# Optimization experiments

Hardware: AMD Instinct MI355X
Metric: run time of the kernel (lower is better)

The kernel has to match this reference:

```python
import jax, jax.numpy as jnp
import numpy as np
from jax import lax

B, N0, N1 = 4, 256, 256
NVOX = N0 * N1
NSUB, NLOR, RAYLEN, NTOF = 8, 32768, 256, 1
NBLK, CH = 4, 16
SUBSETS = np.linspace(0, NSUB, NBLK, endpoint=False).astype(int)  # [0,2,4,6]


def setup_inputs() -> dict:
    key = jax.random.key(0)
    ks = jax.random.split(key, 12)
    osem = jax.random.uniform(ks[0], (B, 1, N0, N1, 1), jnp.float32) + 0.1
    data = jax.random.uniform(ks[1], (B, NSUB, NLOR, NTOF), jnp.float32)
    mult = jax.random.uniform(ks[2], (B, NSUB, NLOR, 1), jnp.float32) + 0.5
    contam = jax.random.uniform(ks[3], (B, NSUB, NLOR, NTOF), jnp.float32) + 0.1
    adjoint_ones = jax.random.uniform(ks[4], (B, NSUB, N0, N1, 1), jnp.float32) + 0.5
    norm = jax.random.uniform(ks[5], (B,), jnp.float32) + 0.5
    ray_idx = jax.random.randint(ks[6], (NSUB, NLOR, RAYLEN), 0, NVOX, dtype=jnp.int32)
    proj_weights = jax.random.uniform(ks[7], (NSUB, NLOR, RAYLEN), jnp.float32) / RAYLEN
    w1 = jax.random.normal(ks[8], (CH, 1, 3, 3), jnp.float32) * 0.05
    b1 = jnp.zeros((CH,), jnp.float32)
    w2 = jax.random.normal(ks[9], (1, CH, 3, 3), jnp.float32) * 0.05
    b2 = jnp.zeros((1,), jnp.float32)
    net_weight = jnp.asarray(1.0, jnp.float32)
    return dict(osem=osem, data=data, multiplicative_corrections=mult,
                contamination=contam, adjoint_ones=adjoint_ones, norm=norm,
                ray_idx=ray_idx, proj_weights=proj_weights,
                w1=w1, b1=b1, w2=w2, b2=b2, net_weight=net_weight)


def _conv(x, w):
    return lax.conv_general_dilated(x, w, (1, 1), 'SAME',
                                    dimension_numbers=('NCHW', 'OIHW', 'NCHW'))


def _net(x, w1, b1, w2, b2):
    # x: (B,1,N0,N1,1) -> treat as NCHW 2D image with 1 channel
    img = x[:, :, :, :, 0]
    h = jax.nn.relu(_conv(img, w1) + b1[None, :, None, None])
    o = _conv(h, w2) + b2[None, :, None, None]
    return o[..., None]


def _fidelity(x, data, mult, contam, adj_ones, norm, ray_idx, pw, subset):
    # unscaled image, flattened: (B, NVOX)
    img_flat = norm[:, None] * x[:, 0, :, :, 0].reshape(B, NVOX)
    ii = ray_idx[subset]          # (NLOR, RAYLEN) voxel indices per ray
    ww = pw[subset]               # (NLOR, RAYLEN) Joseph weights
    # forward projection: gather + weighted sum along each ray
    fwd = jnp.einsum('bls,ls->bl', img_flat[:, ii], ww)[..., None]  # (B,NLOR,1)
    expected = mult[:, subset] * fwd + contam[:, subset]            # (B,NLOR,NTOF)
    ratio = (mult[:, subset] * (1.0 - data[:, subset] / expected)).sum(-1)  # (B,NLOR)
    # adjoint projection: scatter-add along each ray
    back = jnp.zeros((B, NVOX), x.dtype).at[:, ii].add(ww * ratio[:, :, None])
    upd = back * (img_flat / adj_ones[:, subset].reshape(B, NVOX))
    return (upd / norm[:, None]).reshape(B, 1, N0, N1, 1)


def reference(osem, data, multiplicative_corrections, contamination,
              adjoint_ones, norm, ray_idx, proj_weights,
              w1, b1, w2, b2, net_weight):
    x = osem
    for subset in SUBSETS:
        x_data = _fidelity(x, data, multiplicative_corrections, contamination,
                           adjoint_ones, norm, ray_idx, proj_weights, int(subset))
        x_net = _net(x, w1, b1, w2, b2)
        x = jax.nn.relu(osem - x_data + net_weight * x_net)
    return x
```

## Files before the change

kernel.cpp:

```cpp
#include <hip/hip_runtime.h>
#include <hip/hip_fp16.h>

#define BB 4
#define N0 256
#define N1 256
#define NVOX 65536
#define NSUB 8
#define NLOR 32768
#define RAYLEN 256
#define CH 16
#define NPTS (NLOR * RAYLEN)
#define VOXQ 16384
#define VOXT 32768
#define CCH 32

__global__ __launch_bounds__(256) void k_transpose(const float* __restrict__ osem,
                                                   float* __restrict__ xt) {
    int v = blockIdx.x * blockDim.x + threadIdx.x;
    if (v >= NVOX) return;
    float4 o;
    o.x = osem[0 * NVOX + v];
    o.y = osem[1 * NVOX + v];
    o.z = osem[2 * NVOX + v];
    o.w = osem[3 * NVOX + v];
    ((float4*)xt)[v] = o;
}

__device__ __forceinline__ float upk_w(unsigned p) {
    return __half2float(__ushort_as_half((unsigned short)(p >> 16)));
}

__device__ __forceinline__ unsigned pk2(float a, float b) {
    __half2 h = __floats2half2_rn(a, b);
    return *reinterpret_cast<unsigned*>(&h);
}

__global__ __launch_bounds__(256) void k_fwdpack(
    const int* __restrict__ ridx,
    const float* __restrict__ pw,
    const float* __restrict__ xt,
    const float* __restrict__ data,
    const float* __restrict__ mult,
    const float* __restrict__ contam,
    const float* __restrict__ norm,
    float* __restrict__ ratio,
    unsigned* __restrict__ packed)
{
    const int wave = threadIdx.x >> 6;
    const int lane = threadIdx.x & 63;
    const int half = lane >> 5;
    const int sub  = lane & 31;
    const int l = blockIdx.x * 8 + wave * 2 + half;
    const long e0 = (long)l * 64;

    const long ea = e0 + sub;
    const long eb = e0 + sub + 32;

    int4   ida = ((const int4*)ridx)[ea];
    float4 wa  = ((const float4*)pw)[ea];
    int4   idb = ((const int4*)ridx)[eb];
    float4 wb  = ((const float4*)pw)[eb];

    uint4 pka, pkb;
    pka.x = (unsigned)ida.x | ((unsigned)__half_as_ushort(__float2half_rn(wa.x)) << 16);
    pka.y = (unsigned)ida.y | ((unsigned)__half_as_ushort(__float2half_rn(wa.y)) << 16);
    pka.z = (unsigned)ida.z | ((unsigned)__half_as_ushort(__float2half_rn(wa.z)) << 16);
    pka.w = (unsigned)ida.w | ((unsigned)__half_as_ushort(__float2half_rn(wa.w)) << 16);
    pkb.x = (unsigned)idb.x | ((unsigned)__half_as_ushort(__float2half_rn(wb.x)) << 16);
    pkb.y = (unsigned)idb.y | ((unsigned)__half_as_ushort(__float2half_rn(wb.y)) << 16);
    pkb.z = (unsigned)idb.z | ((unsigned)__half_as_ushort(__float2half_rn(wb.z)) << 16);
    pkb.w = (unsigned)idb.w | ((unsigned)__half_as_ushort(__float2half_rn(wb.w)) << 16);
    ((uint4*)packed)[ea] = pka;
    ((uint4*)packed)[eb] = pkb;

    float ax = 0.f, ay = 0.f, az = 0.f, aw = 0.f;
    {
        float4 xv;
        xv = ((const float4*)xt)[ida.x];
        ax += xv.x * wa.x; ay += xv.y * wa.x; az += xv.z * wa.x; aw += xv.w * wa.x;
        xv = ((const float4*)xt)[ida.y];
        ax += xv.x * wa.y; ay += xv.y * wa.y; az += xv.z * wa.y; aw += xv.w * wa.y;
        xv = ((const float4*)xt)[ida.z];
        ax += xv.x * wa.z; ay += xv.y * wa.z; az += xv.z * wa.z; aw += xv.w * wa.z;
        xv = ((const float4*)xt)[ida.w];
        ax += xv.x * wa.w; ay += xv.y * wa.w; az += xv.z * wa.w; aw += xv.w * wa.w;
        xv = ((const float4*)xt)[idb.x];
        ax += xv.x * wb.x; ay += xv.y * wb.x; az += xv.z * wb.x; aw += xv.w * wb.x;
        xv = ((const float4*)xt)[idb.y];
        ax += xv.x * wb.y; ay += xv.y * wb.y; az += xv.z * wb.y; aw += xv.w * wb.y;
        xv = ((const float4*)xt)[idb.z];
        ax += xv.x * wb.z; ay += xv.y * wb.z; az += xv.z * wb.z; aw += xv.w * wb.z;
        xv = ((const float4*)xt)[idb.w];
        ax += xv.x * wb.w; ay += xv.y * wb.w; az += xv.z * wb.w; aw += xv.w * wb.w;
    }
#pragma unroll
    for (int off = 16; off >= 1; off >>= 1) {
        ax += __shfl_xor(ax, off);
        ay += __shfl_xor(ay, off);
        az += __shfl_xor(az, off);
        aw += __shfl_xor(aw, off);
    }
    if (sub == 0) {
        float fwd[4] = {ax, ay, az, aw};
        float rr[4];
#pragma unroll
        for (int b = 0; b < 4; ++b) {
            long o = (long)b * (NSUB * NLOR) + l;
            float m = mult[o];
            float ee = m * (norm[b] * fwd[b]) + contam[o];
            rr[b] = m * (1.0f - data[o] / ee);
        }
        ((float4*)ratio)[l] = make_float4(rr[0], rr[1], rr[2], rr[3]);
    }
}

__global__ __launch_bounds__(1024) void k_back_pk(
    const unsigned* __restrict__ packed,
    const float* __restrict__ ratio,
    unsigned* __restrict__ part,
    int PC)
{
    __shared__ unsigned acc[VOXQ];
    const int c = blockIdx.x;
    const int g = blockIdx.y;
    const int p = g & 1;
    const unsigned lo = (unsigned)(g >> 1) * VOXQ;

    for (int q = threadIdx.x; q < VOXQ; q += 1024) acc[q] = 0u;
    __syncthreads();

    const unsigned abase = (unsigned)(uintptr_t)(&acc[0]);

    const int n4 = PC >> 2;
    const uint4* src = (const uint4*)packed + (size_t)c * n4;
    const float2* rat2 = (const float2*)ratio;
    const int e0 = c * n4;

#define PKADD(u, R)                                                              \
    {                                                                            \
        unsigned q_ = ((u) & 0xffffu) - lo;                                      \
        if (q_ < VOXQ) {                                                         \
            float w_ = upk_w(u);                                                 \
            unsigned d_ = pk2(w_ * (R).x, w_ * (R).y);                           \
            unsigned a_ = abase + (q_ << 2);                                     \
            asm volatile("ds_pk_add_f16 %0, %1" :: "v"(a_), "v"(d_) : "memory"); \
        }                                                                        \
    }
#define PROC(P, R) PKADD(P.x, R) PKADD(P.y, R) PKADD(P.z, R) PKADD(P.w, R)

    for (int base4 = 0; base4 < n4; base4 += 4096) {
        const int ea = base4 + (int)threadIdx.x;
        uint4 A = src[ea];
        uint4 B = src[ea + 1024];
        uint4 C2 = src[ea + 2048];
        uint4 D = src[ea + 3072];
        float2 ra = rat2[(((e0 + ea) >> 6) << 1) + p];
        float2 rb = rat2[(((e0 + ea + 1024) >> 6) << 1) + p];
        float2 rc = rat2[(((e0 + ea + 2048) >> 6) << 1) + p];
        float2 rd = rat2[(((e0 + ea + 3072) >> 6) << 1) + p];
        PROC(A, ra) PROC(B, rb) PROC(C2, rc) PROC(D, rd)
    }
#undef PROC
#undef PKADD

    asm volatile("s_waitcnt lgkmcnt(0)" ::: "memory");
    __syncthreads();

    unsigned* dst = part + ((size_t)c * 2 + p) * NVOX + lo;
    for (int q = threadIdx.x; q < VOXQ; q += 1024) dst[q] = acc[q];
}

__global__ __launch_bounds__(256) void k_reduce(
    const unsigned* __restrict__ part,
    float* __restrict__ back)
{
    const int t = blockIdx.x * 256 + threadIdx.x;
    const int v0 = t * 2;
    const int pr = blockIdx.y;
    float s0 = 0.f, s1 = 0.f, s2 = 0.f, s3 = 0.f;
#pragma unroll
    for (int cc = 0; cc < CCH; ++cc) {
        uint2 u = *(const uint2*)&part[((size_t)cc * 2 + pr) * NVOX + v0];
        s0 += __half2float(__ushort_as_half((unsigned short)(u.x & 0xffffu)));
        s1 += __half2float(__ushort_as_half((unsigned short)(u.x >> 16)));
        s2 += __half2float(__ushort_as_half((unsigned short)(u.y & 0xffffu)));
        s3 += __half2float(__ushort_as_half((unsigned short)(u.y >> 16)));
    }
    ((float2*)back)[(size_t)v0 * 2 + pr] = make_float2(s0, s1);
    ((float2*)back)[(size_t)(v0 + 1) * 2 + pr] = make_float2(s2, s3);
}

#define TI 8
#define TJ 32
__global__ __launch_bounds__(256) void k_net_combine(
    const float* __restrict__ xt_in,
    const float* __restrict__ w1,
    const float* __restrict__ b1,
    const float* __restrict__ w2,
    const float* __restrict__ b2,
    const float* __restrict__ back,
    const float* __restrict__ osem,
    const float* __restrict__ adj,
    const float* __restrict__ nwp,
    float* __restrict__ xt_out,
    float* __restrict__ out_planar)
{
    __shared__ float img[(TI + 4) * (TJ + 4)];
    __shared__ float hsm[8 * (TI + 2) * (TJ + 2)];
    __shared__ float ws1[144], ws2[144], bs1[16];

    const int i0 = blockIdx.x * TI;
    const int j0 = blockIdx.y * TJ;
    const int b  = blockIdx.z;
    const int tid = threadIdx.x;

    if (tid < 144) { ws1[tid] = w1[tid]; ws2[tid] = w2[tid]; }
    if (tid < 16) bs1[tid] = b1[tid];

    for (int q = tid; q < (TI + 4) * (TJ + 4); q += 256) {
        int ii = q / (TJ + 4), jj = q % (TJ + 4);
        int gi = i0 - 2 + ii, gj = j0 - 2 + jj;
        float v = 0.f;
        if (gi >= 0 && gi < N0 && gj >= 0 && gj < N1)
            v = xt_in[(size_t)(gi * N1 + gj) * 4 + b];
        img[q] = v;
    }
    __syncthreads();

    const int li = tid >> 5, lj = tid & 31;
    const int HA = (TI + 2) * (TJ + 2);
    float o = b2[0];

#pragma unroll
    for (int pass = 0; pass < 2; ++pass) {
        for (int q = tid; q < 8 * HA; q += 256) {
            int c8 = q / HA, r = q % HA;
            int c = pass * 8 + c8;
            int ii = r / (TJ + 2), jj = r % (TJ + 2);
            int gi = i0 - 1 + ii, gj = j0 - 1 + jj;
            float hv = 0.f;
            if (gi >= 0 && gi < N0 && gj >= 0 && gj < N1) {
                float a = bs1[c];
#pragma unroll
                for (int di = 0; di < 3; ++di)
#pragma unroll
                    for (int dj = 0; dj < 3; ++dj)
                        a += img[(ii + di) * (TJ + 4) + (jj + dj)] *
                             ws1[c * 9 + di * 3 + dj];
                hv = fmaxf(a, 0.f);
            }
            hsm[q] = hv;
        }
        __syncthreads();
#pragma unroll
        for (int c8 = 0; c8 < 8; ++c8)
#pragma unroll
            for (int di = 0; di < 3; ++di)
#pragma unroll
                for (int dj = 0; dj < 3; ++dj)
                    o += hsm[c8 * HA + (li + di) * (TJ + 2) + (lj + dj)] *
                         ws2[(pass * 8 + c8) * 9 + di * 3 + dj];
        if (pass == 0) __syncthreads();
    }

    const float nw = nwp[0];
    const int pr = b >> 1, hi = b & 1;
    const int v = (i0 + li) * N1 + (j0 + lj);
    float2 bp = ((const float2*)back)[(size_t)v * 2 + pr];
    float bk = hi ? bp.y : bp.x;
    float xv = img[(li + 2) * (TJ + 4) + (lj + 2)];
    float x_data = bk * xv / adj[(size_t)b * NSUB * NVOX + v];
    float xnew = fmaxf(osem[(size_t)b * NVOX + v] - x_data + nw * o, 0.f);
    xt_out[(size_t)v * 4 + b] = xnew;
    if (out_planar) out_planar[(size_t)b * NVOX + v] = xnew;
}

__global__ __launch_bounds__(256) void k_fwd(
    const int* __restrict__ ridx, const float* __restrict__ pw,
    const float* __restrict__ xt, const float* __restrict__ data,
    const float* __restrict__ mult, const float* __restrict__ contam,
    const float* __restrict__ norm, float* __restrict__ ratio)
{
    const int wave = threadIdx.x >> 6;
    const int lane = threadIdx.x & 63;
    const int l = blockIdx.x * 4 + wave;
    const long base = (long)l * RAYLEN;
    float ax = 0.f, ay = 0.f, az = 0.f, aw = 0.f;
#pragma unroll
    for (int k = 0; k < 4; ++k) {
        int r = lane + (k << 6);
        float wt = pw[base + r];
        float4 xv = ((const float4*)xt)[ridx[base + r]];
        ax += xv.x * wt; ay += xv.y * wt; az += xv.z * wt; aw += xv.w * wt;
    }
#pragma unroll
    for (int off = 32; off >= 1; off >>= 1) {
        ax += __shfl_xor(ax, off); ay += __shfl_xor(ay, off);
        az += __shfl_xor(az, off); aw += __shfl_xor(aw, off);
    }
    if (lane == 0) {
        float fwd[4] = {ax, ay, az, aw};
        float rr[4];
#pragma unroll
        for (int b = 0; b < 4; ++b) {
            long o = (long)b * (NSUB * NLOR) + l;
            float m = mult[o];
            float e = m * (norm[b] * fwd[b]) + contam[o];
            rr[b] = m * (1.0f - data[o] / e);
        }
        ((float4*)ratio)[l] = make_float4(rr[0], rr[1], rr[2], rr[3]);
    }
}

__global__ __launch_bounds__(1024) void k_back(
    const int* __restrict__ ridx, const float* __restrict__ pw,
    const float* __restrict__ ratio, float* __restrict__ part, int PC)
{
    __shared__ float acc[VOXT];
    const int c = blockIdx.x;
    const int g = blockIdx.y;
    const int b = g & 3;
    const int lo = (g >> 2) * VOXT;
    for (int q = threadIdx.x; q < VOXT; q += 1024) acc[q] = 0.0f;
    __syncthreads();
    const int pbeg = c * PC;
    const int pend = min(pbeg + PC, NPTS);
#pragma unroll 2
    for (int pt = pbeg + (int)threadIdx.x * 4; pt < pend; pt += 1024 * 4) {
        int4   id = *(const int4*)(ridx + pt);
        float4 w  = *(const float4*)(pw + pt);
        float  r  = ratio[(pt >> 8) * 4 + b];
        unsigned r0 = (unsigned)(id.x - lo), r1 = (unsigned)(id.y - lo);
        unsigned r2 = (unsigned)(id.z - lo), r3 = (unsigned)(id.w - lo);
        if (r0 < VOXT) atomicAdd(&acc[r0], w.x * r);
        if (r1 < VOXT) atomicAdd(&acc[r1], w.y * r);
        if (r2 < VOXT) atomicAdd(&acc[r2], w.z * r);
        if (r3 < VOXT) atomicAdd(&acc[r3], w.w * r);
    }
    __syncthreads();
    float4* dst = (float4*)(part + ((size_t)c * 4 + b) * NVOX + lo);
    const float4* srcl = (const float4*)acc;
    for (int q = threadIdx.x; q < VOXT / 4; q += 1024) dst[q] = srcl[q];
}

__global__ __launch_bounds__(256) void k_conv1(
    const float* __restrict__ xt, const float* __restrict__ w1,
    const float* __restrict__ b1, float* __restrict__ h)
{
    int t = blockIdx.x * blockDim.x + threadIdx.x;
    int b = t >> 16;
    int v = t & 65535;
    int i = v >> 8, j = v & 255;
    float in[3][3];
#pragma unroll
    for (int di = 0; di < 3; ++di)
#pragma unroll
        for (int dj = 0; dj < 3; ++dj) {
            int ii = i + di - 1, jj = j + dj - 1;
            in[di][dj] = (ii >= 0 && ii < N0 && jj >= 0 && jj < N1)
                             ? xt[(size_t)((ii << 8) | jj) * 4 + b]
                             : 0.0f;
        }
    float* hp = h + (size_t)t * CH;
#pragma unroll
    for (int c = 0; c < CH; ++c) {
        float acc = b1[c];
#pragma unroll
        for (int di = 0; di < 3; ++di)
#pragma unroll
            for (int dj = 0; dj < 3; ++dj)
                acc += in[di][dj] * w1[c * 9 + di * 3 + dj];
        hp[c] = fmaxf(acc, 0.0f);
    }
}

__global__ __launch_bounds__(256) void k_combine(
    const float* __restrict__ h, const float* __restrict__ w2,
    const float* __restrict__ b2, const float* __restrict__ part,
    const float* __restrict__ xt_in, const float* __restrict__ osem,
    const float* __restrict__ adj, const float* __restrict__ nwp, int C,
    float* __restrict__ xt_out, float* __restrict__ out_planar)
{
    int t = blockIdx.x * blockDim.x + threadIdx.x;
    int b = t >> 16;
    int v = t & 65535;
    int i = v >> 8, j = v & 255;
    float o = b2[0];
#pragma unroll
    for (int di = 0; di < 3; ++di) {
        int ii = i + di - 1;
        if (ii < 0 || ii >= N0) continue;
#pragma unroll
        for (int dj = 0; dj < 3; ++dj) {
            int jj = j + dj - 1;
            if (jj < 0 || jj >= N1) continue;
            const float* hp = h + ((size_t)b * NVOX + ((ii << 8) | jj)) * CH;
#pragma unroll
            for (int c = 0; c < CH; ++c)
                o += hp[c] * w2[c * 9 + di * 3 + dj];
        }
    }
    float bk = 0.0f;
    for (int c = 0; c < C; ++c)
        bk += part[((size_t)c * 4 + b) * NVOX + v];
    float xv = xt_in[(size_t)v * 4 + b];
    float x_data = bk * xv / adj[(size_t)b * NSUB * NVOX + v];
    float xnew = osem[t] - x_data + nwp[0] * o;
    xnew = fmaxf(xnew, 0.0f);
    xt_out[(size_t)v * 4 + b] = xnew;
    if (out_planar) out_planar[t] = xnew;
}

extern "C" void kernel_launch(void* const* d_in, const int* in_sizes, int n_in,
                              void* d_out, int out_size, void* d_ws, size_t ws_size,
                              hipStream_t stream) {
    const float* osem   = (const float*)d_in[0];
    const float* data   = (const float*)d_in[1];
    const float* mult   = (const float*)d_in[2];
    const float* contam = (const float*)d_in[3];
    const float* adj    = (const float*)d_in[4];
    const float* norm   = (const float*)d_in[5];
    const int*   ray_idx = (const int*)d_in[6];
    const float* pw     = (const float*)d_in[7];
    const float* w1     = (const float*)d_in[8];
    const float* b1     = (const float*)d_in[9];
    const float* w2     = (const float*)d_in[10];
    const float* b2     = (const float*)d_in[11];
    const float* nw     = (const float*)d_in[12];
    float* out = (float*)d_out;

    const size_t MB = 1024 * 1024;
    float* ws  = (float*)d_ws;
    float* xtA = ws;
    float* xtB = ws + (size_t)NVOX * 4;
    const int subsets[4] = {0, 2, 4, 6};

    bool use_pk = (ws_size >= 90 * MB);

    k_transpose<<<NVOX / 256, 256, 0, stream>>>(osem, xtA);

    if (use_pk) {
        const int PC = NPTS / CCH;
        unsigned* part   = (unsigned*)(ws + (size_t)NVOX * 8);
        unsigned* packed = part + (size_t)CCH * 2 * NVOX;
        float*    backv  = (float*)(packed + (size_t)NPTS);
        float*    ratio  = backv + (size_t)NVOX * 4;

        float* xin = xtA;
        float* xout = xtB;
        for (int it = 0; it < 4; ++it) {
            int s = subsets[it];
            k_fwdpack<<<NLOR / 8, 256, 0, stream>>>(
                ray_idx + (size_t)s * NPTS, pw + (size_t)s * NPTS, xin,
                data + (size_t)s * NLOR, mult + (size_t)s * NLOR,
                contam + (size_t)s * NLOR, norm, ratio, packed);
            k_back_pk<<<dim3(CCH, 8), 1024, 0, stream>>>(packed, ratio, part, PC);
            k_reduce<<<dim3(NVOX / 512, 2), 256, 0, stream>>>(part, backv);
            k_net_combine<<<dim3(N0 / TI, N1 / TJ, BB), 256, 0, stream>>>(
                xin, w1, b1, w2, b2, backv, osem,
                adj + (size_t)s * NVOX, nw,
                xout, (it == 3) ? out : nullptr);
            float* tmp = xin; xin = xout; xout = tmp;
        }
    } else {
        int C = (ws_size >= (18 + 32) * MB + NVOX) ? 32
              : (ws_size >= (18 + 16) * MB + NVOX) ? 16 : 8;
        const int PC = NPTS / C;
        float* part = ws + (size_t)NVOX * 8;
        float* h    = part + (size_t)C * NVOX * 4;
        float* ratio = h;

        float* xin = xtA;
        float* xout = xtB;
        for (int it = 0; it < 4; ++it) {
            int s = subsets[it];
            const int*   rs = ray_idx + (size_t)s * NPTS;
            const float* ps = pw + (size_t)s * NPTS;
            k_fwd<<<NLOR / 4, 256, 0, stream>>>(
                rs, ps, xin,
                data + (size_t)s * NLOR, mult + (size_t)s * NLOR,
                contam + (size_t)s * NLOR, norm, ratio);
            k_back<<<dim3(C, 8), 1024, 0, stream>>>(rs, ps, ratio, part, PC);
            k_conv1<<<(BB * NVOX) / 256, 256, 0, stream>>>(xin, w1, b1, h);
            k_combine<<<(BB * NVOX) / 256, 256, 0, stream>>>(
                h, w2, b2, part, xin, osem,
                adj + (size_t)s * NVOX, nw, C,
                xout, (it == 3) ? out : nullptr);
            float* tmp = xin; xin = xout; xout = tmp;
        }
    }
}
```

Measured before the change: 663.0 us.

## Fuse all iteration stages into one persistent kernel with grid-wide barriers

Replaces the per-iteration chain of forward-pack, LDS back-projection, reduce and net-combine kernels with a single persistent kernel of 256×1024-thread blocks. Stages are separated by a hand-rolled atomic grid barrier, and the initial transpose is folded in as well. The aim is to remove the launch gaps and kernel tail effects across the 17 launches. In exchange, the forward gather runs at a fixed occupancy of one 1024-thread block per CU with a loop of 4 rays per wave. The code also assumes every block is co-resident, and the barrier will deadlock if they are not.

```diff
diff --git a/kernel.cpp b/kernel.cpp
--- a/kernel.cpp
+++ b/kernel.cpp
@@ -13,6 +13,291 @@
 #define VOXQ 16384
 #define VOXT 32768
 #define CCH 32
+#define NBLK 256
+#define NTHR 1024
+
+__device__ __forceinline__ float upk_w(unsigned p) {
+    return __half2float(__ushort_as_half((unsigned short)(p >> 16)));
+}
+__device__ __forceinline__ unsigned pk2(float a, float b) {
+    __half2 h = __floats2half2_rn(a, b);
+    return *reinterpret_cast<unsigned*>(&h);
+}
+
+__global__ __launch_bounds__(1024, 4) void k_mega(
+    const float* __restrict__ osem,
+    const float* __restrict__ data,
+    const float* __restrict__ mult,
+    const float* __restrict__ contam,
+    const float* __restrict__ adj,
+    const float* __restrict__ norm,
+    const int*   __restrict__ ray_idx,
+    const float* __restrict__ pw,
+    const float* __restrict__ w1, const float* __restrict__ b1,
+    const float* __restrict__ w2, const float* __restrict__ b2,
+    const float* __restrict__ nwp,
+    float* __restrict__ xtA, float* __restrict__ xtB,
+    unsigned* __restrict__ part,
+    unsigned* __restrict__ packed,
+    float* __restrict__ backv,
+    float* __restrict__ ratio,
+    int* __restrict__ bar,
+    float* __restrict__ out)
+{
+    __shared__ unsigned lds[16384];
+    const int bid = blockIdx.x;
+    const int tid = threadIdx.x;
+    int barph = 0;
+
+    auto gbar = [&]() {
+        __syncthreads();
+        if (tid == 0) {
+            ++barph;
+            __hip_atomic_fetch_add(&bar[0], 1, __ATOMIC_RELEASE,
+                                   __HIP_MEMORY_SCOPE_AGENT);
+            const int target = NBLK * barph;
+            while (__hip_atomic_load(&bar[0], __ATOMIC_RELAXED,
+                                     __HIP_MEMORY_SCOPE_AGENT) < target)
+                __builtin_amdgcn_s_sleep(8);
+            (void)__hip_atomic_load(&bar[0], __ATOMIC_ACQUIRE,
+                                    __HIP_MEMORY_SCOPE_AGENT);
+        }
+        __syncthreads();
+    };
+
+    {
+        int t = bid * NTHR + tid;
+        if (t < NVOX) {
+            float4 o;
+            o.x = osem[t];
+            o.y = osem[NVOX + t];
+            o.z = osem[2 * NVOX + t];
+            o.w = osem[3 * NVOX + t];
+            ((float4*)xtA)[t] = o;
+        }
+    }
+    gbar();
+
+    float* xin = xtA;
+    float* xout = xtB;
+    for (int it = 0; it < 4; ++it) {
+        const int s = it * 2;
+        const int*   rs = ray_idx + (size_t)s * NPTS;
+        const float* ps = pw + (size_t)s * NPTS;
+
+        {
+            const int wv = bid * 16 + (tid >> 6);
+            const int lane = tid & 63;
+            const int half = lane >> 5;
+            const int sub = lane & 31;
+            for (int k = 0; k < 4; ++k) {
+                const int l = wv * 8 + k * 2 + half;
+                const long e0 = (long)l * 64;
+                const long ea = e0 + sub, eb = e0 + sub + 32;
+
+                int4   ida = ((const int4*)rs)[ea];
+                float4 wa  = ((const float4*)ps)[ea];
+                int4   idb = ((const int4*)rs)[eb];
+                float4 wb  = ((const float4*)ps)[eb];
+
+                uint4 pka, pkb;
+                pka.x = (unsigned)ida.x | ((unsigned)__half_as_ushort(__float2half_rn(wa.x)) << 16);
+                pka.y = (unsigned)ida.y | ((unsigned)__half_as_ushort(__float2half_rn(wa.y)) << 16);
+                pka.z = (unsigned)ida.z | ((unsigned)__half_as_ushort(__float2half_rn(wa.z)) << 16);
+                pka.w = (unsigned)ida.w | ((unsigned)__half_as_ushort(__float2half_rn(wa.w)) << 16);
+                pkb.x = (unsigned)idb.x | ((unsigned)__half_as_ushort(__float2half_rn(wb.x)) << 16);
+                pkb.y = (unsigned)idb.y | ((unsigned)__half_as_ushort(__float2half_rn(wb.y)) << 16);
+                pkb.z = (unsigned)idb.z | ((unsigned)__half_as_ushort(__float2half_rn(wb.z)) << 16);
+                pkb.w = (unsigned)idb.w | ((unsigned)__half_as_ushort(__float2half_rn(wb.w)) << 16);
+                ((uint4*)packed)[ea] = pka;
+                ((uint4*)packed)[eb] = pkb;
+
+                float ax = 0.f, ay = 0.f, az = 0.f, aw = 0.f;
+                float4 xv;
+                xv = ((const float4*)xin)[ida.x];
+                ax += xv.x * wa.x; ay += xv.y * wa.x; az += xv.z * wa.x; aw += xv.w * wa.x;
+                xv = ((const float4*)xin)[ida.y];
+                ax += xv.x * wa.y; ay += xv.y * wa.y; az += xv.z * wa.y; aw += xv.w * wa.y;
+                xv = ((const float4*)xin)[ida.z];
+                ax += xv.x * wa.z; ay += xv.y * wa.z; az += xv.z * wa.z; aw += xv.w * wa.z;
+                xv = ((const float4*)xin)[ida.w];
+                ax += xv.x * wa.w; ay += xv.y * wa.w; az += xv.z * wa.w; aw += xv.w * wa.w;
+                xv = ((const float4*)xin)[idb.x];
+                ax += xv.x * wb.x; ay += xv.y * wb.x; az += xv.z * wb.x; aw += xv.w * wb.x;
+                xv = ((const float4*)xin)[idb.y];
+                ax += xv.x * wb.y; ay += xv.y * wb.y; az += xv.z * wb.y; aw += xv.w * wb.y;
+                xv = ((const float4*)xin)[idb.z];
+                ax += xv.x * wb.z; ay += xv.y * wb.z; az += xv.z * wb.z; aw += xv.w * wb.z;
+                xv = ((const float4*)xin)[idb.w];
+                ax += xv.x * wb.w; ay += xv.y * wb.w; az += xv.z * wb.w; aw += xv.w * wb.w;
+
+#pragma unroll
+                for (int off = 16; off >= 1; off >>= 1) {
+                    ax += __shfl_xor(ax, off);
+                    ay += __shfl_xor(ay, off);
+                    az += __shfl_xor(az, off);
+                    aw += __shfl_xor(aw, off);
+                }
+                if (sub == 0) {
+                    float fwd[4] = {ax, ay, az, aw};
+                    float rr[4];
+#pragma unroll
+                    for (int b = 0; b < 4; ++b) {
+                        long o = (long)b * (NSUB * NLOR) + (long)s * NLOR + l;
+                        float m = mult[o];
+                        float ee = m * (norm[b] * fwd[b]) + contam[o];
+                        rr[b] = m * (1.0f - data[o] / ee);
+                    }
+                    ((float4*)ratio)[l] = make_float4(rr[0], rr[1], rr[2], rr[3]);
+                }
+            }
+        }
+        gbar();
+
+        {
+            const int c = bid >> 3;
+            const int g = bid & 7;
+            const int p = g & 1;
+            const unsigned lo = (unsigned)(g >> 1) * VOXQ;
+
+            for (int q = tid; q < VOXQ; q += NTHR) lds[q] = 0u;
+            __syncthreads();
+
+            const unsigned abase = (unsigned)(uintptr_t)(&lds[0]);
+            const int n4 = (NPTS / CCH) >> 2;
+            const uint4* src = (const uint4*)packed + (size_t)c * n4;
+            const float2* rat2 = (const float2*)ratio;
+            const int e0 = c * n4;
+
+#define PKADD(u, R)                                                              \
+    {                                                                            \
+        unsigned q_ = ((u) & 0xffffu) - lo;                                      \
+        if (q_ < VOXQ) {                                                         \
+            float w_ = upk_w(u);                                                 \
+            unsigned d_ = pk2(w_ * (R).x, w_ * (R).y);                           \
+            unsigned a_ = abase + (q_ << 2);                                     \
+            asm volatile("ds_pk_add_f16 %0, %1" :: "v"(a_), "v"(d_) : "memory"); \
+        }                                                                        \
+    }
+#define PROC(P, R) PKADD(P.x, R) PKADD(P.y, R) PKADD(P.z, R) PKADD(P.w, R)
+
+            for (int base4 = 0; base4 < n4; base4 += 4096) {
+                const int ea = base4 + tid;
+                uint4 A = src[ea];
+                uint4 B = src[ea + 1024];
+                uint4 C2 = src[ea + 2048];
+                uint4 D = src[ea + 3072];
+                float2 ra = rat2[(((e0 + ea) >> 6) << 1) + p];
+                float2 rb = rat2[(((e0 + ea + 1024) >> 6) << 1) + p];
+                float2 rc = rat2[(((e0 + ea + 2048) >> 6) << 1) + p];
+                float2 rd = rat2[(((e0 + ea + 3072) >> 6) << 1) + p];
+                PROC(A, ra) PROC(B, rb) PROC(C2, rc) PROC(D, rd)
+            }
+#undef PROC
+#undef PKADD
+            asm volatile("s_waitcnt lgkmcnt(0)" ::: "memory");
+            __syncthreads();
+
+            unsigned* dst = part + ((size_t)c * 2 + p) * NVOX + lo;
+            for (int q = tid; q < VOXQ; q += NTHR) dst[q] = lds[q];
+        }
+        gbar();
+
+        {
+            int t = bid * NTHR + tid;
+            if (t < 2 * NVOX) {
+                int pr = t >> 16;
+                int v = t & 65535;
+                float s0 = 0.f, s1 = 0.f;
+#pragma unroll
+                for (int cc = 0; cc < CCH; ++cc) {
+                    unsigned u = part[((size_t)cc * 2 + pr) * NVOX + v];
+                    s0 += __half2float(__ushort_as_half((unsigned short)(u & 0xffffu)));
+                    s1 += __half2float(__ushort_as_half((unsigned short)(u >> 16)));
+                }
+                ((float2*)backv)[(size_t)v * 2 + pr] = make_float2(s0, s1);
+            }
+        }
+        gbar();
+
+        {
+            const int sb = tid >> 8, stid = tid & 255;
+            const int T = bid * 4 + sb;
+            const int b = T >> 8;
+            const int rem = T & 255;
+            const int i0 = (rem >> 3) * 8;
+            const int j0 = (rem & 7) * 32;
+
+            float* img = (float*)lds + sb * 432;
+            float* hsm = (float*)lds + 1728 + sb * 2720;
+            float* wsh = (float*)lds + 1728 + 4 * 2720;
+            float* ws1 = wsh;
+            float* ws2 = wsh + 144;
+            float* bs1 = wsh + 288;
+            if (tid < 144) { ws1[tid] = w1[tid]; ws2[tid] = w2[tid]; }
+            if (tid < 16) bs1[tid] = b1[tid];
+
+            for (int q = stid; q < 432; q += 256) {
+                int ii = q / 36, jj = q % 36;
+                int gi = i0 - 2 + ii, gj = j0 - 2 + jj;
+                float v = 0.f;
+                if (gi >= 0 && gi < N0 && gj >= 0 && gj < N1)
+                    v = xin[(size_t)(gi * N1 + gj) * 4 + b];
+                img[q] = v;
+            }
+            __syncthreads();
+
+            const int HA = 10 * 34;
+            const int li = stid >> 5, lj = stid & 31;
+            float o = b2[0];
+#pragma unroll
+            for (int pass = 0; pass < 2; ++pass) {
+                for (int q = stid; q < 8 * HA; q += 256) {
+                    int c8 = q / HA, r = q % HA;
+                    int c = pass * 8 + c8;
+                    int ii = r / 34, jj = r % 34;
+                    int gi = i0 - 1 + ii, gj = j0 - 1 + jj;
+                    float hv = 0.f;
+                    if (gi >= 0 && gi < N0 && gj >= 0 && gj < N1) {
+                        float a = bs1[c];
+#pragma unroll
+                        for (int di = 0; di < 3; ++di)
+#pragma unroll
+                            for (int dj = 0; dj < 3; ++dj)
+                                a += img[(ii + di) * 36 + (jj + dj)] *
+                                     ws1[c * 9 + di * 3 + dj];
+                        hv = fmaxf(a, 0.f);
+                    }
+                    hsm[q] = hv;
+                }
+                __syncthreads();
+#pragma unroll
+                for (int c8 = 0; c8 < 8; ++c8)
+#pragma unroll
+                    for (int di = 0; di < 3; ++di)
+#pragma unroll
+                        for (int dj = 0; dj < 3; ++dj)
+                            o += hsm[c8 * HA + (li + di) * 34 + (lj + dj)] *
+                                 ws2[(pass * 8 + c8) * 9 + di * 3 + dj];
+                if (pass == 0) __syncthreads();
+            }
+
+            const float nw = nwp[0];
+            const int pr = b >> 1, hi = b & 1;
+            const int v = (i0 + li) * N1 + (j0 + lj);
+            float2 bp = ((const float2*)backv)[(size_t)v * 2 + pr];
+            float bk = hi ? bp.y : bp.x;
+            float xv = img[(li + 2) * 36 + (lj + 2)];
+            float x_data = bk * xv / adj[(size_t)b * NSUB * NVOX + (size_t)s * NVOX + v];
+            float xnew = fmaxf(osem[(size_t)b * NVOX + v] - x_data + nw * o, 0.f);
+            xout[(size_t)v * 4 + b] = xnew;
+            if (it == 3) out[(size_t)b * NVOX + v] = xnew;
+        }
+        gbar();
+
+        float* tmp = xin; xin = xout; xout = tmp;
+    }
+}
 
 __global__ __launch_bounds__(256) void k_transpose(const float* __restrict__ osem,
                                                    float* __restrict__ xt) {
@@ -24,255 +309,6 @@
     o.z = osem[2 * NVOX + v];
     o.w = osem[3 * NVOX + v];
     ((float4*)xt)[v] = o;
-}
-
-__device__ __forceinline__ float upk_w(unsigned p) {
-    return __half2float(__ushort_as_half((unsigned short)(p >> 16)));
-}
-
-__device__ __forceinline__ unsigned pk2(float a, float b) {
-    __half2 h = __floats2half2_rn(a, b);
-    return *reinterpret_cast<unsigned*>(&h);
-}
-
-__global__ __launch_bounds__(256) void k_fwdpack(
-    const int* __restrict__ ridx,
-    const float* __restrict__ pw,
-    const float* __restrict__ xt,
-    const float* __restrict__ data,
-    const float* __restrict__ mult,
-    const float* __restrict__ contam,
-    const float* __restrict__ norm,
-    float* __restrict__ ratio,
-    unsigned* __restrict__ packed)
-{
-    const int wave = threadIdx.x >> 6;
-    const int lane = threadIdx.x & 63;
-    const int half = lane >> 5;
-    const int sub  = lane & 31;
-    const int l = blockIdx.x * 8 + wave * 2 + half;
-    const long e0 = (long)l * 64;
-
-    const long ea = e0 + sub;
-    const long eb = e0 + sub + 32;
-
-    int4   ida = ((const int4*)ridx)[ea];
-    float4 wa  = ((const float4*)pw)[ea];
-    int4   idb = ((const int4*)ridx)[eb];
-    float4 wb  = ((const float4*)pw)[eb];
-
-    uint4 pka, pkb;
-    pka.x = (unsigned)ida.x | ((unsigned)__half_as_ushort(__float2half_rn(wa.x)) << 16);
-    pka.y = (unsigned)ida.y | ((unsigned)__half_as_ushort(__float2half_rn(wa.y)) << 16);
-    pka.z = (unsigned)ida.z | ((unsigned)__half_as_ushort(__float2half_rn(wa.z)) << 16);
-    pka.w = (unsigned)ida.w | ((unsigned)__half_as_ushort(__float2half_rn(wa.w)) << 16);
-    pkb.x = (unsigned)idb.x | ((unsigned)__half_as_ushort(__float2half_rn(wb.x)) << 16);
-    pkb.y = (unsigned)idb.y | ((unsigned)__half_as_ushort(__float2half_rn(wb.y)) << 16);
-    pkb.z = (unsigned)idb.z | ((unsigned)__half_as_ushort(__float2half_rn(wb.z)) << 16);
-    pkb.w = (unsigned)idb.w | ((unsigned)__half_as_ushort(__float2half_rn(wb.w)) << 16);
-    ((uint4*)packed)[ea] = pka;
-    ((uint4*)packed)[eb] = pkb;
-
-    float ax = 0.f, ay = 0.f, az = 0.f, aw = 0.f;
-    {
-        float4 xv;
-        xv = ((const float4*)xt)[ida.x];
-        ax += xv.x * wa.x; ay += xv.y * wa.x; az += xv.z * wa.x; aw += xv.w * wa.x;
-        xv = ((const float4*)xt)[ida.y];
-        ax += xv.x * wa.y; ay += xv.y * wa.y; az += xv.z * wa.y; aw += xv.w * wa.y;
-        xv = ((const float4*)xt)[ida.z];
-        ax += xv.x * wa.z; ay += xv.y * wa.z; az += xv.z * wa.z; aw += xv.w * wa.z;
-        xv = ((const float4*)xt)[ida.w];
-        ax += xv.x * wa.w; ay += xv.y * wa.w; az += xv.z * wa.w; aw += xv.w * wa.w;
-        xv = ((const float4*)xt)[idb.x];
-        ax += xv.x * wb.x; ay += xv.y * wb.x; az += xv.z * wb.x; aw += xv.w * wb.x;
-        xv = ((const float4*)xt)[idb.y];
-        ax += xv.x * wb.y; ay += xv.y * wb.y; az += xv.z * wb.y; aw += xv.w * wb.y;
-        xv = ((const float4*)xt)[idb.z];
-        ax += xv.x * wb.z; ay += xv.y * wb.z; az += xv.z * wb.z; aw += xv.w * wb.z;
-        xv = ((const float4*)xt)[idb.w];
-        ax += xv.x * wb.w; ay += xv.y * wb.w; az += xv.z * wb.w; aw += xv.w * wb.w;
-    }
-#pragma unroll
-    for (int off = 16; off >= 1; off >>= 1) {
-        ax += __shfl_xor(ax, off);
-        ay += __shfl_xor(ay, off);
-        az += __shfl_xor(az, off);
-        aw += __shfl_xor(aw, off);
-    }
-    if (sub == 0) {
-        float fwd[4] = {ax, ay, az, aw};
-        float rr[4];
-#pragma unroll
-        for (int b = 0; b < 4; ++b) {
-            long o = (long)b * (NSUB * NLOR) + l;
-            float m = mult[o];
-            float ee = m * (norm[b] * fwd[b]) + contam[o];
-            rr[b] = m * (1.0f - data[o] / ee);
-        }
-        ((float4*)ratio)[l] = make_float4(rr[0], rr[1], rr[2], rr[3]);
-    }
-}
-
-__global__ __launch_bounds__(1024) void k_back_pk(
-    const unsigned* __restrict__ packed,
-    const float* __restrict__ ratio,
-    unsigned* __restrict__ part,
-    int PC)
-{
-    __shared__ unsigned acc[VOXQ];
-    const int c = blockIdx.x;
-    const int g = blockIdx.y;
-    const int p = g & 1;
-    const unsigned lo = (unsigned)(g >> 1) * VOXQ;
-
-    for (int q = threadIdx.x; q < VOXQ; q += 1024) acc[q] = 0u;
-    __syncthreads();
-
-    const unsigned abase = (unsigned)(uintptr_t)(&acc[0]);
-
-    const int n4 = PC >> 2;
-    const uint4* src = (const uint4*)packed + (size_t)c * n4;
-    const float2* rat2 = (const float2*)ratio;
-    const int e0 = c * n4;
-
-#define PKADD(u, R)                                                              \
-    {                                                                            \
-        unsigned q_ = ((u) & 0xffffu) - lo;                                      \
-        if (q_ < VOXQ) {                                                         \
-            float w_ = upk_w(u);                                                 \
-            unsigned d_ = pk2(w_ * (R).x, w_ * (R).y);                           \
-            unsigned a_ = abase + (q_ << 2);                                     \
-            asm volatile("ds_pk_add_f16 %0, %1" :: "v"(a_), "v"(d_) : "memory"); \
-        }                                                                        \
-    }
-#define PROC(P, R) PKADD(P.x, R) PKADD(P.y, R) PKADD(P.z, R) PKADD(P.w, R)
-
-    for (int base4 = 0; base4 < n4; base4 += 4096) {
-        const int ea = base4 + (int)threadIdx.x;
-        uint4 A = src[ea];
-        uint4 B = src[ea + 1024];
-        uint4 C2 = src[ea + 2048];
-        uint4 D = src[ea + 3072];
-        float2 ra = rat2[(((e0 + ea) >> 6) << 1) + p];
-        float2 rb = rat2[(((e0 + ea + 1024) >> 6) << 1) + p];
-        float2 rc = rat2[(((e0 + ea + 2048) >> 6) << 1) + p];
-        float2 rd = rat2[(((e0 + ea + 3072) >> 6) << 1) + p];
-        PROC(A, ra) PROC(B, rb) PROC(C2, rc) PROC(D, rd)
-    }
-#undef PROC
-#undef PKADD
-
-    asm volatile("s_waitcnt lgkmcnt(0)" ::: "memory");
-    __syncthreads();
-
-    unsigned* dst = part + ((size_t)c * 2 + p) * NVOX + lo;
-    for (int q = threadIdx.x; q < VOXQ; q += 1024) dst[q] = acc[q];
-}
-
-__global__ __launch_bounds__(256) void k_reduce(
-    const unsigned* __restrict__ part,
-    float* __restrict__ back)
-{
-    const int t = blockIdx.x * 256 + threadIdx.x;
-    const int v0 = t * 2;
-    const int pr = blockIdx.y;
-    float s0 = 0.f, s1 = 0.f, s2 = 0.f, s3 = 0.f;
-#pragma unroll
-    for (int cc = 0; cc < CCH; ++cc) {
-        uint2 u = *(const uint2*)&part[((size_t)cc * 2 + pr) * NVOX + v0];
-        s0 += __half2float(__ushort_as_half((unsigned short)(u.x & 0xffffu)));
-        s1 += __half2float(__ushort_as_half((unsigned short)(u.x >> 16)));
-        s2 += __half2float(__ushort_as_half((unsigned short)(u.y & 0xffffu)));
-        s3 += __half2float(__ushort_as_half((unsigned short)(u.y >> 16)));
-    }
-    ((float2*)back)[(size_t)v0 * 2 + pr] = make_float2(s0, s1);
-    ((float2*)back)[(size_t)(v0 + 1) * 2 + pr] = make_float2(s2, s3);
-}
-
-#define TI 8
-#define TJ 32
-__global__ __launch_bounds__(256) void k_net_combine(
-    const float* __restrict__ xt_in,
-    const float* __restrict__ w1,
-    const float* __restrict__ b1,
-    const float* __restrict__ w2,
-    const float* __restrict__ b2,
-    const float* __restrict__ back,
-    const float* __restrict__ osem,
-    const float* __restrict__ adj,
-    const float* __restrict__ nwp,
-    float* __restrict__ xt_out,
-    float* __restrict__ out_planar)
-{
-    __shared__ float img[(TI + 4) * (TJ + 4)];
-    __shared__ float hsm[8 * (TI + 2) * (TJ + 2)];
-    __shared__ float ws1[144], ws2[144], bs1[16];
-
-    const int i0 = blockIdx.x * TI;
-    const int j0 = blockIdx.y * TJ;
-    const int b  = blockIdx.z;
-    const int tid = threadIdx.x;
-
-    if (tid < 144) { ws1[tid] = w1[tid]; ws2[tid] = w2[tid]; }
-    if (tid < 16) bs1[tid] = b1[tid];
-
-    for (int q = tid; q < (TI + 4) * (TJ + 4); q += 256) {
-        int ii = q / (TJ + 4), jj = q % (TJ + 4);
-        int gi = i0 - 2 + ii, gj = j0 - 2 + jj;
-        float v = 0.f;
-        if (gi >= 0 && gi < N0 && gj >= 0 && gj < N1)
-            v = xt_in[(size_t)(gi * N1 + gj) * 4 + b];
-        img[q] = v;
-    }
-    __syncthreads();
-
-    const int li = tid >> 5, lj = tid & 31;
-    const int HA = (TI + 2) * (TJ + 2);
-    float o = b2[0];
-
-#pragma unroll
-    for (int pass = 0; pass < 2; ++pass) {
-        for (int q = tid; q < 8 * HA; q += 256) {
-            int c8 = q / HA, r = q % HA;
-            int c = pass * 8 + c8;
-            int ii = r / (TJ + 2), jj = r % (TJ + 2);
-            int gi = i0 - 1 + ii, gj = j0 - 1 + jj;
-            float hv = 0.f;
-            if (gi >= 0 && gi < N0 && gj >= 0 && gj < N1) {
-                float a = bs1[c];
-#pragma unroll
-                for (int di = 0; di < 3; ++di)
-#pragma unroll
-                    for (int dj = 0; dj < 3; ++dj)
-                        a += img[(ii + di) * (TJ + 4) + (jj + dj)] *
-                             ws1[c * 9 + di * 3 + dj];
-                hv = fmaxf(a, 0.f);
-            }
-            hsm[q] = hv;
-        }
-        __syncthreads();
-#pragma unroll
-        for (int c8 = 0; c8 < 8; ++c8)
-#pragma unroll
-            for (int di = 0; di < 3; ++di)
-#pragma unroll
-                for (int dj = 0; dj < 3; ++dj)
-                    o += hsm[c8 * HA + (li + di) * (TJ + 2) + (lj + dj)] *
-                         ws2[(pass * 8 + c8) * 9 + di * 3 + dj];
-        if (pass == 0) __syncthreads();
-    }
-
-    const float nw = nwp[0];
-    const int pr = b >> 1, hi = b & 1;
-    const int v = (i0 + li) * N1 + (j0 + lj);
-    float2 bp = ((const float2*)back)[(size_t)v * 2 + pr];
-    float bk = hi ? bp.y : bp.x;
-    float xv = img[(li + 2) * (TJ + 4) + (lj + 2)];
-    float x_data = bk * xv / adj[(size_t)b * NSUB * NVOX + v];
-    float xnew = fmaxf(osem[(size_t)b * NVOX + v] - x_data + nw * o, 0.f);
-    xt_out[(size_t)v * 4 + b] = xnew;
-    if (out_planar) out_planar[(size_t)b * NVOX + v] = xnew;
 }
 
 __global__ __launch_bounds__(256) void k_fwd(
@@ -431,44 +467,35 @@
 
     const size_t MB = 1024 * 1024;
     float* ws  = (float*)d_ws;
-    float* xtA = ws;
-    float* xtB = ws + (size_t)NVOX * 4;
-    const int subsets[4] = {0, 2, 4, 6};
-
-    bool use_pk = (ws_size >= 90 * MB);
-
-    k_transpose<<<NVOX / 256, 256, 0, stream>>>(osem, xtA);
-
-    if (use_pk) {
-        const int PC = NPTS / CCH;
-        unsigned* part   = (unsigned*)(ws + (size_t)NVOX * 8);
+
+    bool use_mega = (ws_size >= 90 * MB);
+
+    if (use_mega) {
+        float*    xtA    = ws;
+        float*    xtB    = xtA + (size_t)NVOX * 4;
+        unsigned* part   = (unsigned*)(xtB + (size_t)NVOX * 4);
         unsigned* packed = part + (size_t)CCH * 2 * NVOX;
         float*    backv  = (float*)(packed + (size_t)NPTS);
         float*    ratio  = backv + (size_t)NVOX * 4;
-
-        float* xin = xtA;
-        float* xout = xtB;
-        for (int it = 0; it < 4; ++it) {
-            int s = subsets[it];
-            k_fwdpack<<<NLOR / 8, 256, 0, stream>>>(
-                ray_idx + (size_t)s * NPTS, pw + (size_t)s * NPTS, xin,
-                data + (size_t)s * NLOR, mult + (size_t)s * NLOR,
-                contam + (size_t)s * NLOR, norm, ratio, packed);
-            k_back_pk<<<dim3(CCH, 8), 1024, 0, stream>>>(packed, ratio, part, PC);
-            k_reduce<<<dim3(NVOX / 512, 2), 256, 0, stream>>>(part, backv);
-            k_net_combine<<<dim3(N0 / TI, N1 / TJ, BB), 256, 0, stream>>>(
-                xin, w1, b1, w2, b2, backv, osem,
-                adj + (size_t)s * NVOX, nw,
-                xout, (it == 3) ? out : nullptr);
-            float* tmp = xin; xin = xout; xout = tmp;
-        }
+        int*      bar    = (int*)(ratio + (size_t)NLOR * 4);
+
+        hipMemsetAsync(bar, 0, 2 * sizeof(int), stream);
+        k_mega<<<NBLK, NTHR, 0, stream>>>(
+            osem, data, mult, contam, adj, norm, ray_idx, pw,
+            w1, b1, w2, b2, nw,
+            xtA, xtB, part, packed, backv, ratio, bar, out);
     } else {
+        float* xtA = ws;
+        float* xtB = ws + (size_t)NVOX * 4;
+        const int subsets[4] = {0, 2, 4, 6};
         int C = (ws_size >= (18 + 32) * MB + NVOX) ? 32
               : (ws_size >= (18 + 16) * MB + NVOX) ? 16 : 8;
         const int PC = NPTS / C;
         float* part = ws + (size_t)NVOX * 8;
         float* h    = part + (size_t)C * NVOX * 4;
         float* ratio = h;
+
+        k_transpose<<<NVOX / 256, 256, 0, stream>>>(osem, xtA);
 
         float* xin = xtA;
         float* xout = xtB;
```

Result: slower. 1.217 ms (+83.6%).
